# Kernel optimization log

Measured on AMD Instinct MI355X. Metric: run time of the kernel, lower is better.

## Reference

```python
import jax, jax.numpy as jnp
import numpy as np

B, S, D, H = 2, 2048, 1024, 16
HD = D // H  # 64
ROPE_BASE = 1024.0


def _rope_tables(seq_len, head_dim, dtype=jnp.float32):
    # inv_freq over head_dim//4 frequencies, padded with zeros to head_dim//2
    inv_freq = (1.0 / ROPE_BASE) ** jnp.linspace(0.0, 1.0, head_dim // 4, dtype=dtype)
    inv_freq = jnp.concatenate([inv_freq, jnp.zeros(head_dim // 4, dtype=dtype)])
    pos = jnp.arange(seq_len, dtype=dtype)
    ang = pos[:, None] * inv_freq[None, :]  # [S, HD//2]
    return jnp.sin(ang), jnp.cos(ang)


def _apply_rope(t, sin, cos):
    # t: [B, H, S, HD]; sin/cos: [S, HD//2]
    t1, t2 = jnp.split(t, 2, axis=-1)
    sin = sin[None, None, :, :]
    cos = cos[None, None, :, :]
    return jnp.concatenate([t1 * cos - t2 * sin, t1 * sin + t2 * cos], axis=-1)


def setup_inputs() -> dict:
    key = jax.random.key(0)
    ks = jax.random.split(key, 6)
    std = 0.02
    x = jax.random.normal(ks[0], (B, S, D), dtype=jnp.float32)
    Wq = jax.random.normal(ks[1], (D, D), dtype=jnp.float32) * std
    Wk = jax.random.normal(ks[2], (D, D), dtype=jnp.float32) * std
    Wv = jax.random.normal(ks[3], (D, D), dtype=jnp.float32) * std
    Wo = jax.random.normal(ks[4], (D, D), dtype=jnp.float32) * std
    bo = jnp.zeros((D,), dtype=jnp.float32)
    # causal block mask (standard create_block_mask causal pattern)
    mask = jnp.tril(jnp.ones((S, S), dtype=bool))
    return {"x": x, "Wq": Wq, "Wk": Wk, "Wv": Wv, "Wo": Wo, "bo": bo, "mask": mask}


def reference(x, Wq, Wk, Wv, Wo, bo, mask):
    b, s, d = x.shape
    h, hd = H, d // H
    # torch Linear: y = x @ W.T
    q = (x @ Wq.T).reshape(b, s, h, hd).transpose(0, 2, 1, 3)
    k = (x @ Wk.T).reshape(b, s, h, hd).transpose(0, 2, 1, 3)
    v = (x @ Wv.T).reshape(b, s, h, hd).transpose(0, 2, 1, 3)
    sin, cos = _rope_tables(s, hd, dtype=x.dtype)
    q = _apply_rope(q, sin, cos)
    k = _apply_rope(k, sin, cos)
    scale = 1.0 / jnp.sqrt(jnp.asarray(hd, dtype=x.dtype))
    scores = jnp.einsum('bhqd,bhkd->bhqk', q, k) * scale
    scores = jnp.where(mask[None, None, :, :], scores, -jnp.inf)
    attn = jax.nn.softmax(scores, axis=-1)
    out = jnp.einsum('bhqk,bhkd->bhqd', attn, v)
    out = out.transpose(0, 2, 1, 3).reshape(b, s, d)
    return out @ Wo.T + bo
```

## Files before the change

kernel.cpp:

```cpp
#include <hip/hip_runtime.h>
#include <hip/hip_bf16.h>
#include <stdint.h>

typedef _Float16 f16;
typedef __attribute__((ext_vector_type(8))) _Float16 f16x8;
typedef __attribute__((ext_vector_type(4))) float f32x4;

constexpr int Bb = 2, Ss = 2048, Dd = 1024, Hh = 16, HDim = 64;

#define MFMA16(a, b, c) __builtin_amdgcn_mfma_f32_16x16x32_f16(a, b, c, 0, 0, 0)
#define GLDS(g, l) __builtin_amdgcn_global_load_lds( \
    (const __attribute__((address_space(1))) void*)(g), \
    (__attribute__((address_space(3))) void*)(l), 16, 0, 0)

__global__ void k_cvt5(const float* __restrict__ x,
                       const float* __restrict__ w0, const float* __restrict__ w1,
                       const float* __restrict__ w2, const float* __restrict__ w3,
                       f16* __restrict__ xo, f16* __restrict__ o0, f16* __restrict__ o1,
                       f16* __restrict__ o2, f16* __restrict__ o3,
                       float* __restrict__ sinT, float* __restrict__ cosT) {
    const int z = blockIdx.y;
    if (z == 5) {
        int i = blockIdx.x * blockDim.x + threadIdx.x;
        if (i < 32768) {
            int s = i >> 4, j = i & 15;
            float ang = (float)s * exp2f(-10.0f * (float)j / 15.0f);
            sinT[i] = sinf(ang);
            cosT[i] = cosf(ang);
        }
        return;
    }
    const float* in; f16* out; int n8;
    switch (z) {
        case 0: in = x;  out = xo; n8 = 524288; break;
        case 1: in = w0; out = o0; n8 = 131072; break;
        case 2: in = w1; out = o1; n8 = 131072; break;
        case 3: in = w2; out = o2; n8 = 131072; break;
        default: in = w3; out = o3; n8 = 131072; break;
    }
    for (int i = blockIdx.x * blockDim.x + threadIdx.x; i < n8;
         i += gridDim.x * blockDim.x) {
        float4 a = ((const float4*)in)[2 * i];
        float4 b = ((const float4*)in)[2 * i + 1];
        f16x8 o = {(f16)a.x, (f16)a.y, (f16)a.z, (f16)a.w,
                   (f16)b.x, (f16)b.y, (f16)b.z, (f16)b.w};
        ((f16x8*)out)[i] = o;
    }
}

__global__ __launch_bounds__(256) void k_gemm(
    const f16* __restrict__ A,
    const f16* __restrict__ B0, const f16* __restrict__ B1, const f16* __restrict__ B2,
    void* C0, void* C1, void* C2,
    const float* __restrict__ sinT, const float* __restrict__ cosT, int K) {
    __shared__ f16 As[2][128 * 32];
    __shared__ f16 Bs[2][128 * 32];

    const int wg = blockIdx.x;
    const int xcd = wg & 7, slot = wg >> 3;
    const int mg = xcd >> 1, ng = xcd & 1;
    const int m = mg * 8 + (slot & 7);
    const int nzi = ng * 12 + (slot >> 3);
    const int z = nzi >> 3;
    const int m0 = m * 128, n0 = (nzi & 7) * 128;
    const f16* Bt = (z == 0) ? B0 : (z == 1) ? B1 : B2;
    void* Cout    = (z == 0) ? C0 : (z == 1) ? C1 : C2;

    const int tid = threadIdx.x;
    const int w = tid >> 6, l = tid & 63;
    const int l15 = l & 15, l4 = l >> 4;
    const int wr = w >> 1, wc = w & 1;

    f32x4 acc[4][4] = {};

    const int f0 = tid, row0 = f0 >> 2, cb0 = ((f0 & 3) * 16) ^ ((row0 & 3) << 4);
    const int f1 = 256 + tid, row1 = f1 >> 2, cb1 = ((f1 & 3) * 16) ^ ((row1 & 3) << 4);
    const char* gA0 = (const char*)(A + (size_t)(m0 + row0) * K) + cb0;
    const char* gA1 = (const char*)(A + (size_t)(m0 + row1) * K) + cb1;
    const char* gB0 = (const char*)(Bt + (size_t)(n0 + row0) * K) + cb0;
    const char* gB1 = (const char*)(Bt + (size_t)(n0 + row1) * K) + cb1;
    const int ld0 = (w * 64) * 16, ld1 = (256 + w * 64) * 16;

#define STAGE(kt, buf)                                        \
    do {                                                      \
        GLDS(gA0 + (size_t)(kt) * 2, (char*)As[buf] + ld0);   \
        GLDS(gA1 + (size_t)(kt) * 2, (char*)As[buf] + ld1);   \
        GLDS(gB0 + (size_t)(kt) * 2, (char*)Bs[buf] + ld0);   \
        GLDS(gB1 + (size_t)(kt) * 2, (char*)Bs[buf] + ld1);   \
    } while (0)

    STAGE(0, 0);
    for (int kt = 0; kt < K; kt += 32) {
        const int cur = (kt >> 5) & 1;
        __syncthreads();
        if (kt + 32 < K) STAGE(kt + 32, cur ^ 1);

        f16x8 af[4], bfr[4];
#pragma unroll
        for (int mf = 0; mf < 4; ++mf) {
            int r = wr * 64 + mf * 16 + l15;
            int byo = r * 64 + ((l4 * 16) ^ ((r & 3) << 4));
            af[mf] = *(const f16x8*)((const char*)As[cur] + byo);
        }
#pragma unroll
        for (int nf = 0; nf < 4; ++nf) {
            int r = wc * 64 + nf * 16 + l15;
            int byo = r * 64 + ((l4 * 16) ^ ((r & 3) << 4));
            bfr[nf] = *(const f16x8*)((const char*)Bs[cur] + byo);
        }
#pragma unroll
        for (int mf = 0; mf < 4; ++mf)
#pragma unroll
            for (int nf = 0; nf < 4; ++nf)
                acc[mf][nf] = MFMA16(af[mf], bfr[nf], acc[mf][nf]);
    }
#undef STAGE

    if (z < 2) {
#pragma unroll
        for (int mf = 0; mf < 4; ++mf) {
#pragma unroll
            for (int r = 0; r < 4; ++r) {
                int row = m0 + wr * 64 + mf * 16 + l4 * 4 + r;
                int s = row & (Ss - 1);
                float cs = cosT[(s << 4) + l15];
                float sn = sinT[(s << 4) + l15];
                float t1 = acc[mf][0][r], t2 = acc[mf][2][r];
                acc[mf][0][r] = t1 * cs - t2 * sn;
                acc[mf][2][r] = t1 * sn + t2 * cs;
            }
        }
    }

#pragma unroll
    for (int mf = 0; mf < 4; ++mf)
#pragma unroll
        for (int nf = 0; nf < 4; ++nf) {
            int col = n0 + wc * 64 + nf * 16 + l15;
#pragma unroll
            for (int r = 0; r < 4; ++r) {
                int row = m0 + wr * 64 + mf * 16 + l4 * 4 + r;
                ((f16*)Cout)[(size_t)row * 1024 + col] = (f16)acc[mf][nf][r];
            }
        }
}

__global__ __launch_bounds__(256) void k_gemmo(
    const f16* __restrict__ A, const f16* __restrict__ Bt,
    float* __restrict__ C, const float* __restrict__ bias, int K) {
    __shared__ f16 As[2][64 * 32];
    __shared__ f16 Bs[2][128 * 32];

    const int wg = blockIdx.x;
    const int xcd = wg & 7, slot = wg >> 3;
    const int m0 = (xcd * 8 + (slot & 7)) * 64;
    const int n0 = (slot >> 3) * 128;

    const int tid = threadIdx.x;
    const int w = tid >> 6, l = tid & 63;
    const int l15 = l & 15, l4 = l >> 4;
    const int wr = w >> 1, wc = w & 1;

    f32x4 acc[2][4] = {};

    const int rowA = tid >> 2, cbA = ((tid & 3) * 16) ^ ((rowA & 3) << 4);
    const char* gA = (const char*)(A + (size_t)(m0 + rowA) * K) + cbA;
    const int ldA = tid * 16;
    const int f0 = tid, rowB0 = f0 >> 2, cb0 = ((f0 & 3) * 16) ^ ((rowB0 & 3) << 4);
    const int f1 = 256 + tid, rowB1 = f1 >> 2, cb1 = ((f1 & 3) * 16) ^ ((rowB1 & 3) << 4);
    const char* gB0 = (const char*)(Bt + (size_t)(n0 + rowB0) * K) + cb0;
    const char* gB1 = (const char*)(Bt + (size_t)(n0 + rowB1) * K) + cb1;
    const int ld0 = (w * 64) * 16, ld1 = (256 + w * 64) * 16;

#define STG(kt, buf)                                         \
    do {                                                     \
        GLDS(gA + (size_t)(kt) * 2, (char*)As[buf] + ldA);   \
        GLDS(gB0 + (size_t)(kt) * 2, (char*)Bs[buf] + ld0);  \
        GLDS(gB1 + (size_t)(kt) * 2, (char*)Bs[buf] + ld1);  \
    } while (0)

    STG(0, 0);
    for (int kt = 0; kt < K; kt += 32) {
        const int cur = (kt >> 5) & 1;
        __syncthreads();
        if (kt + 32 < K) STG(kt + 32, cur ^ 1);

        f16x8 af[2], bfr[4];
#pragma unroll
        for (int mf = 0; mf < 2; ++mf) {
            int r = wr * 32 + mf * 16 + l15;
            int byo = r * 64 + ((l4 * 16) ^ ((r & 3) << 4));
            af[mf] = *(const f16x8*)((const char*)As[cur] + byo);
        }
#pragma unroll
        for (int nf = 0; nf < 4; ++nf) {
            int r = wc * 64 + nf * 16 + l15;
            int byo = r * 64 + ((l4 * 16) ^ ((r & 3) << 4));
            bfr[nf] = *(const f16x8*)((const char*)Bs[cur] + byo);
        }
#pragma unroll
        for (int mf = 0; mf < 2; ++mf)
#pragma unroll
            for (int nf = 0; nf < 4; ++nf)
                acc[mf][nf] = MFMA16(af[mf], bfr[nf], acc[mf][nf]);
    }
#undef STG

#pragma unroll
    for (int mf = 0; mf < 2; ++mf)
#pragma unroll
        for (int nf = 0; nf < 4; ++nf) {
            int col = n0 + wc * 64 + nf * 16 + l15;
#pragma unroll
            for (int r = 0; r < 4; ++r) {
                int row = m0 + wr * 32 + mf * 16 + l4 * 4 + r;
                C[(size_t)row * 1024 + col] = acc[mf][nf][r] + bias[col];
            }
        }
}

__global__ __launch_bounds__(256) void k_attn(const f16* __restrict__ Q,
                                              const f16* __restrict__ Kk,
                                              const f16* __restrict__ V,
                                              f16* __restrict__ O) {
    __shared__ f16 Ks[64 * 72];
    __shared__ uint32_t Vt32[64 * 36];
    __shared__ f16 Ps[4 * 16 * 72];

    const int tid = threadIdx.x, w = tid >> 6, l = tid & 63;
    const int l15 = l & 15, l4 = l >> 4;
    const int qi = 31 - (int)blockIdx.y;
    const int q0 = qi * 64;
    const int bh = blockIdx.x, b = bh >> 4, h = bh & 15;
    const size_t rowbase = (size_t)b * Ss * Dd + (size_t)h * HDim;
    const f16* kbase = Kk + rowbase;
    const f16* vbase = V + rowbase;

    const int qb = q0 + w * 16;
    f16x8 aq0, aq1;
    {
        const f16* qp = Q + rowbase + (size_t)(qb + l15) * Dd;
        aq0 = *(const f16x8*)(qp + l4 * 8);
        aq1 = *(const f16x8*)(qp + 32 + l4 * 8);
        const f16 c2 = (f16)0.18033688f;
#pragma unroll
        for (int j = 0; j < 8; ++j) { aq0[j] *= c2; aq1[j] *= c2; }
    }

    f32x4 o[4] = {};
    f32x4 osum = {};
    const f16x8 ones = {(f16)1.f, (f16)1.f, (f16)1.f, (f16)1.f,
                        (f16)1.f, (f16)1.f, (f16)1.f, (f16)1.f};

    const int srow = tid >> 2, sc0 = (tid & 3) * 16;
    const int kvp = tid >> 3, dg = tid & 7;
    const int ntiles = qi + 1;
    f16* Pw = Ps + w * (16 * 72);

    f16x8 k8a = *(const f16x8*)(kbase + (size_t)srow * Dd + sc0);
    f16x8 k8b = *(const f16x8*)(kbase + (size_t)srow * Dd + sc0 + 8);
    f16x8 v8a = *(const f16x8*)(vbase + (size_t)(2 * kvp) * Dd + dg * 8);
    f16x8 v8b = *(const f16x8*)(vbase + (size_t)(2 * kvp + 1) * Dd + dg * 8);

    for (int kt = 0; kt < ntiles; ++kt) {
        const int kv0 = kt * 64;
        __syncthreads();
        *(f16x8*)(Ks + srow * 72 + sc0)     = k8a;
        *(f16x8*)(Ks + srow * 72 + sc0 + 8) = k8b;
        {
            union { f16x8 f; uint16_t u[8]; } ua{v8a}, ub{v8b};
            const int csw = kvp ^ ((dg & 3) << 3);
#pragma unroll
            for (int d = 0; d < 8; ++d) {
                uint32_t val = (uint32_t)ua.u[d] | ((uint32_t)ub.u[d] << 16);
                Vt32[(dg * 8 + d) * 36 + csw] = val;
            }
        }
        __syncthreads();

        if (kt + 1 < ntiles) {
            k8a = *(const f16x8*)(kbase + (size_t)(kv0 + 64 + srow) * Dd + sc0);
            k8b = *(const f16x8*)(kbase + (size_t)(kv0 + 64 + srow) * Dd + sc0 + 8);
            v8a = *(const f16x8*)(vbase + (size_t)(kv0 + 64 + 2 * kvp) * Dd + dg * 8);
            v8b = *(const f16x8*)(vbase + (size_t)(kv0 + 64 + 2 * kvp + 1) * Dd + dg * 8);
        }

        f32x4 sf[4] = {};
#pragma unroll
        for (int kvf = 0; kvf < 4; ++kvf) {
            const f16x8 b0 = *(const f16x8*)(Ks + (kvf * 16 + l15) * 72 + l4 * 8);
            const f16x8 b1 = *(const f16x8*)(Ks + (kvf * 16 + l15) * 72 + 32 + l4 * 8);
            sf[kvf] = MFMA16(aq0, b0, sf[kvf]);
            sf[kvf] = MFMA16(aq1, b1, sf[kvf]);
        }

        const int xpw = l4 << 3;
        if (kt + 1 < ntiles) {
#pragma unroll
            for (int kvf = 0; kvf < 4; ++kvf) {
                const int cw = ((8 * kvf + (l15 >> 1)) ^ xpw) * 2 + (l15 & 1);
#pragma unroll
                for (int r = 0; r < 4; ++r)
                    Pw[(l4 * 4 + r) * 72 + cw] =
                        (f16)__builtin_amdgcn_exp2f(sf[kvf][r]);
            }
        } else {
#pragma unroll
            for (int kvf = 0; kvf < 4; ++kvf) {
                const int kv = kv0 + kvf * 16 + l15;
                const int cw = ((8 * kvf + (l15 >> 1)) ^ xpw) * 2 + (l15 & 1);
#pragma unroll
                for (int r = 0; r < 4; ++r) {
                    float p = __builtin_amdgcn_exp2f(sf[kvf][r]);
                    if (kv > qb + l4 * 4 + r) p = 0.f;
                    Pw[(l4 * 4 + r) * 72 + cw] = (f16)p;
                }
            }
        }

        const int xpr = ((l15 >> 2) & 3) << 3;
        const f16x8 pa0 = *(const f16x8*)(Pw + l15 * 72 + ((l4 * 4) ^ xpr) * 2);
        const f16x8 pa1 = *(const f16x8*)(Pw + l15 * 72 + ((l4 * 4 + 16) ^ xpr) * 2);
#pragma unroll
        for (int df = 0; df < 4; ++df) {
            const int xvr = ((2 * df + (l15 >> 3)) & 3) << 3;
            const int rb = (df * 16 + l15) * 36;
            const f16x8 bv0 = *(const f16x8*)(Vt32 + rb + ((l4 * 4) ^ xvr));
            const f16x8 bv1 = *(const f16x8*)(Vt32 + rb + ((l4 * 4 + 16) ^ xvr));
            o[df] = MFMA16(pa0, bv0, o[df]);
            o[df] = MFMA16(pa1, bv1, o[df]);
        }
        osum = MFMA16(pa0, ones, osum);
        osum = MFMA16(pa1, ones, osum);
    }

#pragma unroll
    for (int r = 0; r < 4; ++r) {
        const float inv = 1.0f / osum[r];
        const int qs = qb + l4 * 4 + r;
        f16* op = O + (size_t)(b * Ss + qs) * Dd + h * HDim + l15;
#pragma unroll
        for (int df = 0; df < 4; ++df) op[df * 16] = (f16)(o[df][r] * inv);
    }
}

extern "C" void kernel_launch(void* const* d_in, const int* in_sizes, int n_in,
                              void* d_out, int out_size, void* d_ws, size_t ws_size,
                              hipStream_t stream) {
    const float* x  = (const float*)d_in[0];
    const float* Wq = (const float*)d_in[1];
    const float* Wk = (const float*)d_in[2];
    const float* Wv = (const float*)d_in[3];
    const float* Wo = (const float*)d_in[4];
    const float* bo = (const float*)d_in[5];

    char* ws = (char*)d_ws;
    f16* x16  = (f16*)(ws);
    f16* a16  = (f16*)(ws);
    f16* q16  = (f16*)(ws + (8u << 20));
    f16* k16  = (f16*)(ws + (16u << 20));
    f16* v16  = (f16*)(ws + (24u << 20));
    f16* wq16 = (f16*)(ws + (32u << 20));
    f16* wk16 = (f16*)(ws + (34u << 20));
    f16* wv16 = (f16*)(ws + (36u << 20));
    f16* wo16 = (f16*)(ws + (38u << 20));
    float* sinT = (float*)(ws + (40u << 20));
    float* cosT = (float*)(ws + (40u << 20) + (128u << 10));

    k_cvt5<<<dim3(512, 6), 256, 0, stream>>>(x, Wq, Wk, Wv, Wo,
                                             x16, wq16, wk16, wv16, wo16,
                                             sinT, cosT);

    k_gemm<<<768, 256, 0, stream>>>(x16, wq16, wk16, wv16,
                                    (void*)q16, (void*)k16, (void*)v16,
                                    sinT, cosT, 1024);

    k_attn<<<dim3(32, 32), 256, 0, stream>>>(q16, k16, v16, a16);

    k_gemmo<<<512, 256, 0, stream>>>(a16, wo16, (float*)d_out, bo, 1024);
}
```

Baseline: 113.3 us.

## Keep attention probabilities in registers via permlane swaps instead of LDS round-trip

```diff
diff --git a/kernel.cpp b/kernel.cpp
--- a/kernel.cpp
+++ b/kernel.cpp
@@ -4,7 +4,9 @@
 
 typedef _Float16 f16;
 typedef __attribute__((ext_vector_type(8))) _Float16 f16x8;
+typedef __attribute__((ext_vector_type(2))) __fp16 fp16x2;
 typedef __attribute__((ext_vector_type(4))) float f32x4;
+typedef __attribute__((ext_vector_type(2))) unsigned int u32x2;
 
 constexpr int Bb = 2, Ss = 2048, Dd = 1024, Hh = 16, HDim = 64;
 
@@ -225,7 +227,6 @@
                                               f16* __restrict__ O) {
     __shared__ f16 Ks[64 * 72];
     __shared__ uint32_t Vt32[64 * 36];
-    __shared__ f16 Ps[4 * 16 * 72];
 
     const int tid = threadIdx.x, w = tid >> 6, l = tid & 63;
     const int l15 = l & 15, l4 = l >> 4;
@@ -255,7 +256,6 @@
     const int srow = tid >> 2, sc0 = (tid & 3) * 16;
     const int kvp = tid >> 3, dg = tid & 7;
     const int ntiles = qi + 1;
-    f16* Pw = Ps + w * (16 * 72);
 
     f16x8 k8a = *(const f16x8*)(kbase + (size_t)srow * Dd + sc0);
     f16x8 k8b = *(const f16x8*)(kbase + (size_t)srow * Dd + sc0 + 8);
@@ -290,37 +290,41 @@
         for (int kvf = 0; kvf < 4; ++kvf) {
             const f16x8 b0 = *(const f16x8*)(Ks + (kvf * 16 + l15) * 72 + l4 * 8);
             const f16x8 b1 = *(const f16x8*)(Ks + (kvf * 16 + l15) * 72 + 32 + l4 * 8);
-            sf[kvf] = MFMA16(aq0, b0, sf[kvf]);
-            sf[kvf] = MFMA16(aq1, b1, sf[kvf]);
-        }
-
-        const int xpw = l4 << 3;
-        if (kt + 1 < ntiles) {
-#pragma unroll
-            for (int kvf = 0; kvf < 4; ++kvf) {
-                const int cw = ((8 * kvf + (l15 >> 1)) ^ xpw) * 2 + (l15 & 1);
-#pragma unroll
-                for (int r = 0; r < 4; ++r)
-                    Pw[(l4 * 4 + r) * 72 + cw] =
-                        (f16)__builtin_amdgcn_exp2f(sf[kvf][r]);
-            }
-        } else {
-#pragma unroll
-            for (int kvf = 0; kvf < 4; ++kvf) {
-                const int kv = kv0 + kvf * 16 + l15;
-                const int cw = ((8 * kvf + (l15 >> 1)) ^ xpw) * 2 + (l15 & 1);
-#pragma unroll
-                for (int r = 0; r < 4; ++r) {
-                    float p = __builtin_amdgcn_exp2f(sf[kvf][r]);
-                    if (kv > qb + l4 * 4 + r) p = 0.f;
-                    Pw[(l4 * 4 + r) * 72 + cw] = (f16)p;
-                }
-            }
-        }
-
-        const int xpr = ((l15 >> 2) & 3) << 3;
-        const f16x8 pa0 = *(const f16x8*)(Pw + l15 * 72 + ((l4 * 4) ^ xpr) * 2);
-        const f16x8 pa1 = *(const f16x8*)(Pw + l15 * 72 + ((l4 * 4 + 16) ^ xpr) * 2);
+            sf[kvf] = MFMA16(b0, aq0, sf[kvf]);
+            sf[kvf] = MFMA16(b1, aq1, sf[kvf]);
+        }
+
+        const bool lastt = (kt + 1 == ntiles);
+        uint32_t D[4][2];
+#pragma unroll
+        for (int kvf = 0; kvf < 4; ++kvf) {
+            float p[4];
+#pragma unroll
+            for (int r = 0; r < 4; ++r) {
+                p[r] = __builtin_amdgcn_exp2f(sf[kvf][r]);
+                if (lastt && (16 * kvf + 4 * l4 + r > w * 16 + l15)) p[r] = 0.f;
+            }
+            union { fp16x2 f; uint32_t u; } c0, c1;
+            c0.f = __builtin_amdgcn_cvt_pkrtz(p[0], p[1]);
+            c1.f = __builtin_amdgcn_cvt_pkrtz(p[2], p[3]);
+            D[kvf][0] = c0.u;
+            D[kvf][1] = c1.u;
+        }
+
+        union { uint32_t u[4]; f16x8 v; } pa0u, pa1u;
+#pragma unroll
+        for (int j = 0; j < 2; ++j) {
+            u32x2 t0 = __builtin_amdgcn_permlane32_swap(D[0][j], D[1][j], false, false);
+            u32x2 u0 = __builtin_amdgcn_permlane16_swap(t0.x, t0.y, false, false);
+            pa0u.u[j]     = u0.x;
+            pa0u.u[j + 2] = u0.y;
+            u32x2 t1 = __builtin_amdgcn_permlane32_swap(D[2][j], D[3][j], false, false);
+            u32x2 u1 = __builtin_amdgcn_permlane16_swap(t1.x, t1.y, false, false);
+            pa1u.u[j]     = u1.x;
+            pa1u.u[j + 2] = u1.y;
+        }
+        const f16x8 pa0 = pa0u.v, pa1 = pa1u.v;
+
 #pragma unroll
         for (int df = 0; df < 4; ++df) {
             const int xvr = ((2 * df + (l15 >> 3)) & 3) << 3;
```

Result: faster. 104.5 us (-7.8%).

## Rewrite causal attention with 32x32 MFMA, in-register P via permlane, larger Q tiles

Applied to the files above, without the earlier changes.

```diff
diff --git a/kernel.cpp b/kernel.cpp
--- a/kernel.cpp
+++ b/kernel.cpp
@@ -4,11 +4,15 @@
 
 typedef _Float16 f16;
 typedef __attribute__((ext_vector_type(8))) _Float16 f16x8;
+typedef __attribute__((ext_vector_type(2))) __fp16 fp16x2;
 typedef __attribute__((ext_vector_type(4))) float f32x4;
+typedef __attribute__((ext_vector_type(16))) float f32x16;
+typedef __attribute__((ext_vector_type(2))) unsigned int u32x2;
 
 constexpr int Bb = 2, Ss = 2048, Dd = 1024, Hh = 16, HDim = 64;
 
 #define MFMA16(a, b, c) __builtin_amdgcn_mfma_f32_16x16x32_f16(a, b, c, 0, 0, 0)
+#define MFMA32(a, b, c) __builtin_amdgcn_mfma_f32_32x32x16_f16(a, b, c, 0, 0, 0)
 #define GLDS(g, l) __builtin_amdgcn_global_load_lds( \
     (const __attribute__((address_space(1))) void*)(g), \
     (__attribute__((address_space(3))) void*)(l), 16, 0, 0)
@@ -223,39 +227,39 @@
                                               const f16* __restrict__ Kk,
                                               const f16* __restrict__ V,
                                               f16* __restrict__ O) {
-    __shared__ f16 Ks[64 * 72];
+    __shared__ f16 Ks[64 * 64];
     __shared__ uint32_t Vt32[64 * 36];
-    __shared__ f16 Ps[4 * 16 * 72];
+    __shared__ float Rs[4][32];
 
     const int tid = threadIdx.x, w = tid >> 6, l = tid & 63;
-    const int l15 = l & 15, l4 = l >> 4;
-    const int qi = 31 - (int)blockIdx.y;
-    const int q0 = qi * 64;
-    const int bh = blockIdx.x, b = bh >> 4, h = bh & 15;
-    const size_t rowbase = (size_t)b * Ss * Dd + (size_t)h * HDim;
+    const int l31 = l & 31, hf = l >> 5;
+    const int qi = 15 - (int)blockIdx.y;
+    const int q0 = qi * 128;
+    const int bh = blockIdx.x, b = bh >> 4, hh = bh & 15;
+    const size_t rowbase = (size_t)b * Ss * Dd + (size_t)hh * HDim;
     const f16* kbase = Kk + rowbase;
     const f16* vbase = V + rowbase;
-
-    const int qb = q0 + w * 16;
-    f16x8 aq0, aq1;
+    const int qw = q0 + w * 32;
+
+    f16x8 aq[4];
     {
-        const f16* qp = Q + rowbase + (size_t)(qb + l15) * Dd;
-        aq0 = *(const f16x8*)(qp + l4 * 8);
-        aq1 = *(const f16x8*)(qp + 32 + l4 * 8);
+        const f16* qp = Q + rowbase + (size_t)(qw + l31) * Dd + hf * 8;
         const f16 c2 = (f16)0.18033688f;
 #pragma unroll
-        for (int j = 0; j < 8; ++j) { aq0[j] *= c2; aq1[j] *= c2; }
-    }
-
-    f32x4 o[4] = {};
-    f32x4 osum = {};
-    const f16x8 ones = {(f16)1.f, (f16)1.f, (f16)1.f, (f16)1.f,
-                        (f16)1.f, (f16)1.f, (f16)1.f, (f16)1.f};
+        for (int s = 0; s < 4; ++s) {
+            aq[s] = *(const f16x8*)(qp + s * 16);
+#pragma unroll
+            for (int j = 0; j < 8; ++j) aq[s][j] *= c2;
+        }
+    }
+
+    f32x16 o0 = {}, o1 = {};
+    float rs = 0.f;
 
     const int srow = tid >> 2, sc0 = (tid & 3) * 16;
+    const int ksw = (srow & 7) << 3;
     const int kvp = tid >> 3, dg = tid & 7;
-    const int ntiles = qi + 1;
-    f16* Pw = Ps + w * (16 * 72);
+    const int ntiles = 2 * qi + 2;
 
     f16x8 k8a = *(const f16x8*)(kbase + (size_t)srow * Dd + sc0);
     f16x8 k8b = *(const f16x8*)(kbase + (size_t)srow * Dd + sc0 + 8);
@@ -265,16 +269,15 @@
     for (int kt = 0; kt < ntiles; ++kt) {
         const int kv0 = kt * 64;
         __syncthreads();
-        *(f16x8*)(Ks + srow * 72 + sc0)     = k8a;
-        *(f16x8*)(Ks + srow * 72 + sc0 + 8) = k8b;
+        *(f16x8*)(Ks + srow * 64 + (sc0 ^ ksw))       = k8a;
+        *(f16x8*)(Ks + srow * 64 + ((sc0 + 8) ^ ksw)) = k8b;
         {
             union { f16x8 f; uint16_t u[8]; } ua{v8a}, ub{v8b};
             const int csw = kvp ^ ((dg & 3) << 3);
 #pragma unroll
-            for (int d = 0; d < 8; ++d) {
-                uint32_t val = (uint32_t)ua.u[d] | ((uint32_t)ub.u[d] << 16);
-                Vt32[(dg * 8 + d) * 36 + csw] = val;
-            }
+            for (int d = 0; d < 8; ++d)
+                Vt32[(dg * 8 + d) * 36 + csw] =
+                    (uint32_t)ua.u[d] | ((uint32_t)ub.u[d] << 16);
         }
         __syncthreads();
 
@@ -285,62 +288,79 @@
             v8b = *(const f16x8*)(vbase + (size_t)(kv0 + 64 + 2 * kvp + 1) * Dd + dg * 8);
         }
 
-        f32x4 sf[4] = {};
-#pragma unroll
-        for (int kvf = 0; kvf < 4; ++kvf) {
-            const f16x8 b0 = *(const f16x8*)(Ks + (kvf * 16 + l15) * 72 + l4 * 8);
-            const f16x8 b1 = *(const f16x8*)(Ks + (kvf * 16 + l15) * 72 + 32 + l4 * 8);
-            sf[kvf] = MFMA16(aq0, b0, sf[kvf]);
-            sf[kvf] = MFMA16(aq1, b1, sf[kvf]);
-        }
-
-        const int xpw = l4 << 3;
-        if (kt + 1 < ntiles) {
-#pragma unroll
-            for (int kvf = 0; kvf < 4; ++kvf) {
-                const int cw = ((8 * kvf + (l15 >> 1)) ^ xpw) * 2 + (l15 & 1);
-#pragma unroll
-                for (int r = 0; r < 4; ++r)
-                    Pw[(l4 * 4 + r) * 72 + cw] =
-                        (f16)__builtin_amdgcn_exp2f(sf[kvf][r]);
-            }
-        } else {
-#pragma unroll
-            for (int kvf = 0; kvf < 4; ++kvf) {
-                const int kv = kv0 + kvf * 16 + l15;
-                const int cw = ((8 * kvf + (l15 >> 1)) ^ xpw) * 2 + (l15 & 1);
-#pragma unroll
-                for (int r = 0; r < 4; ++r) {
-                    float p = __builtin_amdgcn_exp2f(sf[kvf][r]);
-                    if (kv > qb + l4 * 4 + r) p = 0.f;
-                    Pw[(l4 * 4 + r) * 72 + cw] = (f16)p;
+#pragma unroll
+        for (int c = 0; c < 2; ++c) {
+            const int kvc = kv0 + 32 * c;
+            if (kvc > qw) continue;
+            const bool masked = (kvc == qw);
+
+            f32x16 sf = {};
+            const int krow = c * 32 + l31;
+            const int kk = (krow & 7) << 3;
+#pragma unroll
+            for (int s = 0; s < 4; ++s) {
+                const f16x8 ak = *(const f16x8*)(Ks + krow * 64 +
+                                                 ((s * 16 + hf * 8) ^ kk));
+                sf = MFMA32(ak, aq[s], sf);
+            }
+
+            uint32_t Dw[8];
+#pragma unroll
+            for (int rr = 0; rr < 8; ++rr) {
+                float p0 = __builtin_amdgcn_exp2f(sf[2 * rr]);
+                float p1 = __builtin_amdgcn_exp2f(sf[2 * rr + 1]);
+                if (masked) {
+                    const int k0 = ((2 * rr) & 3) + 8 * ((2 * rr) >> 2) + 4 * hf;
+                    if (k0 > l31)     p0 = 0.f;
+                    if (k0 + 1 > l31) p1 = 0.f;
                 }
-            }
-        }
-
-        const int xpr = ((l15 >> 2) & 3) << 3;
-        const f16x8 pa0 = *(const f16x8*)(Pw + l15 * 72 + ((l4 * 4) ^ xpr) * 2);
-        const f16x8 pa1 = *(const f16x8*)(Pw + l15 * 72 + ((l4 * 4 + 16) ^ xpr) * 2);
-#pragma unroll
-        for (int df = 0; df < 4; ++df) {
-            const int xvr = ((2 * df + (l15 >> 3)) & 3) << 3;
-            const int rb = (df * 16 + l15) * 36;
-            const f16x8 bv0 = *(const f16x8*)(Vt32 + rb + ((l4 * 4) ^ xvr));
-            const f16x8 bv1 = *(const f16x8*)(Vt32 + rb + ((l4 * 4 + 16) ^ xvr));
-            o[df] = MFMA16(pa0, bv0, o[df]);
-            o[df] = MFMA16(pa1, bv1, o[df]);
-        }
-        osum = MFMA16(pa0, ones, osum);
-        osum = MFMA16(pa1, ones, osum);
-    }
-
-#pragma unroll
-    for (int r = 0; r < 4; ++r) {
-        const float inv = 1.0f / osum[r];
-        const int qs = qb + l4 * 4 + r;
-        f16* op = O + (size_t)(b * Ss + qs) * Dd + h * HDim + l15;
-#pragma unroll
-        for (int df = 0; df < 4; ++df) op[df * 16] = (f16)(o[df][r] * inv);
+                rs += p0 + p1;
+                union { fp16x2 f; uint32_t u; } cc;
+                cc.f = __builtin_amdgcn_cvt_pkrtz(p0, p1);
+                Dw[rr] = cc.u;
+            }
+
+            union { uint32_t u[4]; f16x8 v; } fr0, fr1;
+            {
+                u32x2 s0 = __builtin_amdgcn_permlane32_swap(Dw[0], Dw[2], false, false);
+                u32x2 s1 = __builtin_amdgcn_permlane32_swap(Dw[1], Dw[3], false, false);
+                fr0.u[0] = s0.x; fr0.u[1] = s1.x; fr0.u[2] = s0.y; fr0.u[3] = s1.y;
+                u32x2 s2 = __builtin_amdgcn_permlane32_swap(Dw[4], Dw[6], false, false);
+                u32x2 s3 = __builtin_amdgcn_permlane32_swap(Dw[5], Dw[7], false, false);
+                fr1.u[0] = s2.x; fr1.u[1] = s3.x; fr1.u[2] = s2.y; fr1.u[3] = s3.y;
+            }
+
+#pragma unroll
+            for (int db = 0; db < 2; ++db) {
+                const int vrow = db * 32 + l31;
+                const int vkey = ((vrow >> 3) & 3) << 3;
+                const f16x8 bv0 = *(const f16x8*)(Vt32 + vrow * 36 +
+                                                  ((c * 16 + hf * 4) ^ vkey));
+                const f16x8 bv1 = *(const f16x8*)(Vt32 + vrow * 36 +
+                                                  ((c * 16 + 8 + hf * 4) ^ vkey));
+                if (db == 0) {
+                    o0 = MFMA32(fr0.v, bv0, o0);
+                    o0 = MFMA32(fr1.v, bv1, o0);
+                } else {
+                    o1 = MFMA32(fr0.v, bv0, o1);
+                    o1 = MFMA32(fr1.v, bv1, o1);
+                }
+            }
+        }
+    }
+
+    rs += __shfl_xor(rs, 32);
+    if (l < 32) Rs[w][l31] = rs;
+    __syncthreads();
+
+#pragma unroll
+    for (int rr = 0; rr < 16; ++rr) {
+        const int ql = (rr & 3) + 8 * (rr >> 2) + 4 * hf;
+        const float inv = 1.0f / Rs[w][ql];
+        const int qs = qw + ql;
+        f16* op = O + (size_t)(b * Ss + qs) * Dd + hh * HDim + l31;
+        op[0]  = (f16)(o0[rr] * inv);
+        op[32] = (f16)(o1[rr] * inv);
     }
 }
 
@@ -375,7 +395,7 @@
                                     (void*)q16, (void*)k16, (void*)v16,
                                     sinT, cosT, 1024);
 
-    k_attn<<<dim3(32, 32), 256, 0, stream>>>(q16, k16, v16, a16);
+    k_attn<<<dim3(32, 16), 256, 0, stream>>>(q16, k16, v16, a16);
 
     k_gemmo<<<512, 256, 0, stream>>>(a16, wo16, (float*)d_out, bo, 1024);
 }
```

Measured after the change: 107.9 us. 4.7% less time.
